# Kernel optimization log

Measured on AMD Instinct MI355X. Metric: run time of the kernel, lower is better.

Reference implementation:

```python
import jax, jax.numpy as jnp
import numpy as np


def _rotary_matrix(m, d):
    """Dense block-diagonal rotary matrix R[m, d, d], faithful to the source
    including the (i-1) exponent quirk."""
    d2 = d // 2
    i = jnp.arange(d2, dtype=jnp.float32)
    theta = 10000.0 ** (-2.0 * (i - 1.0) / d)          # note: (i-1), as in source
    ang = jnp.arange(m, dtype=jnp.float32)[:, None] * theta[None, :]  # [m, d2]
    cos, sin = jnp.cos(ang), jnp.sin(ang)
    ev = 2 * jnp.arange(d2)
    od = ev + 1
    R = jnp.zeros((m, d, d), dtype=jnp.float32)
    R = R.at[:, ev, ev].set(cos)
    R = R.at[:, ev, od].set(-sin)
    R = R.at[:, od, ev].set(sin)
    R = R.at[:, od, od].set(cos)
    return R


def setup_inputs() -> dict:
    key = jax.random.key(0)
    kx, kq, kk, kv = jax.random.split(key, 4)
    B, M, D = 4, 1024, 512
    scale = 1.0 / np.float32(np.sqrt(D))
    x = jax.random.normal(kx, (B, M, D), dtype=jnp.float32)
    w_q = jax.random.normal(kq, (D, D), dtype=jnp.float32) * scale
    w_k = jax.random.normal(kk, (D, D), dtype=jnp.float32) * scale
    w_v = jax.random.normal(kv, (D, D), dtype=jnp.float32) * scale
    R = _rotary_matrix(M, D)  # [M, D, D], ~1 GB, constant (requires_grad=False)
    return {"x": x, "w_q": w_q, "w_k": w_k, "w_v": w_v, "R": R}


def reference(x, w_q, w_k, w_v, R):
    b, m, d = x.shape
    # nn.Linear(d, d, bias=False): y = x @ W.T
    q = jnp.einsum('bmd,ed->bme', x, w_q)
    k = jnp.einsum('bmd,ed->bme', x, w_k)
    v = jnp.einsum('bmd,ed->bme', x, w_v)
    # dense per-position rotary bmm: torch.bmm(q.transpose(0,1), R[:m]).transpose(0,1)
    q_rot = jnp.einsum('bmd,mde->bme', q, R[:m])
    k_rot = jnp.einsum('bmd,mde->bme', k, R[:m])
    # F.scaled_dot_product_attention WITHOUT mask (no is_causal in source);
    # dropout_p=0.1 omitted (deterministic / eval-mode reference)
    scores = jnp.einsum('bqd,bkd->bqk', q_rot, k_rot) / np.float32(np.sqrt(d))
    attn = jax.nn.softmax(scores, axis=-1)
    return jnp.einsum('bqk,bkd->bqd', attn, v)
```

## Files before the change

### kernel.cpp

```cpp
#include <hip/hip_runtime.h>
#include <hip/hip_bf16.h>

#define BB 4
#define MM 1024
#define DD 512
#define MT (BB*MM)

typedef __bf16  bf16x8 __attribute__((ext_vector_type(8)));
typedef float   f32x4  __attribute__((ext_vector_type(4)));

typedef __attribute__((address_space(1))) const unsigned char gas_char;
typedef __attribute__((address_space(3))) unsigned char las_char;

__device__ __forceinline__ void gl_lds16(const void* g, void* l){
    __builtin_amdgcn_global_load_lds((gas_char*)g, (las_char*)l, 16, 0, 0);
}

__device__ __forceinline__ float bf2f(ushort u){
    union{float f; unsigned u;} x; x.u = (unsigned)u << 16; return x.f;
}
__device__ __forceinline__ ushort f2bf(float f){
    union{float f; unsigned u;} x; x.f = f;
    unsigned r = x.u + 0x7FFF + ((x.u >> 16) & 1);
    return (ushort)(r >> 16);
}

__device__ __forceinline__ int detect_bf16(const ushort* __restrict__ x){
    int lane = threadIdx.x & 63;
    ushort u = x[2*lane];
    int e = (u >> 7) & 0xFF;
    bool sane = (e >= 114 && e <= 140);
    unsigned long long b = __ballot(sane);
    return (__popcll(b) >= 48) ? 1 : 0;
}

__device__ __forceinline__ uint4 ld8(const void* __restrict__ base, size_t eidx, int fl){
    if (fl) return ((const uint4*)base)[eidx >> 3];
    const float4* f = (const float4*)base + (eidx >> 2);
    float4 a = f[0], b = f[1];
    uint4 o;
    o.x = (uint)f2bf(a.x) | ((uint)f2bf(a.y) << 16);
    o.y = (uint)f2bf(a.z) | ((uint)f2bf(a.w) << 16);
    o.z = (uint)f2bf(b.x) | ((uint)f2bf(b.y) << 16);
    o.w = (uint)f2bf(b.z) | ((uint)f2bf(b.w) << 16);
    return o;
}

template<int ROWS, int WAVES>
__device__ __forceinline__ void stage_tile(const ushort* __restrict__ g, int ldel,
                                           char* lds, int wid, int lane){
    const int rr = wid*8 + (lane >> 3);
    const int sc = ((lane & 7) ^ (lane >> 3)) * 8;
    #pragma unroll
    for (int r = 0; r < ROWS; r += WAVES*8)
        gl_lds16(g + (size_t)(r + rr)*ldel + sc, lds + (size_t)(r + wid*8)*128);
}

__device__ __forceinline__ bf16x8 frag(const char* lds, int row, int c16){
    return *(const bf16x8*)(lds + row*128 + (((c16) ^ (row & 7)) << 4));
}

__global__ void k_cs(const void* __restrict__ R, const void* __restrict__ x,
                     const void* __restrict__ wq, const void* __restrict__ wk,
                     const void* __restrict__ wv,
                     float2* __restrict__ cs, ushort* __restrict__ xb,
                     ushort* __restrict__ w3b){
    const int fl = detect_bf16((const ushort*)x);
    const int m = blockIdx.x, i = threadIdx.x;
    float c, s;
    if (fl){
        const ushort* Rb = (const ushort*)R;
        size_t base = (size_t)m * DD * DD;
        c = bf2f(Rb[base + (size_t)(2*i)   * DD + 2*i]);
        s = bf2f(Rb[base + (size_t)(2*i+1) * DD + 2*i]);
    } else {
        float ex = -((float)i - 1.0f) * (1.0f/256.0f);
        float th = expf(ex * 9.210340371976184f);
        float ang = (float)m * th;
        c = cosf(ang); s = sinf(ang);
    }
    cs[m*256 + i] = make_float2(c, s);

    size_t chunk = (size_t)m*256 + i;
    ((uint4*)xb)[chunk] = ld8(x, chunk*8, fl);

    if (m < 384){
        const void* W = (m < 128) ? wq : (m < 256) ? wk : wv;
        ushort* dst = w3b + (size_t)(m >> 7) * DD * DD;
        size_t ch = (size_t)(m & 127)*256 + i;
        ((uint4*)dst)[ch] = ld8(W, ch*8, fl);
    }
}

__launch_bounds__(256, 2)
__global__ void k_qkv(const ushort* __restrict__ xb, const ushort* __restrict__ w3b,
                      const float2* __restrict__ cs,
                      ushort* __restrict__ qr, ushort* __restrict__ kr,
                      ushort* __restrict__ vt){
    const int lin = blockIdx.x;
    const int swz = (lin & 7) * 96 + (lin >> 3);
    const int tm  = swz / 24;
    const int rm  = swz % 24;
    const int mat = rm >> 3;
    const int tn  = rm & 7;

    const ushort* A  = xb  + (size_t)(tm*128)*DD;
    const ushort* Bw = w3b + (size_t)mat*DD*DD + (size_t)(tn*64)*DD;

    const int t = threadIdx.x, lane = t & 63, wid = t >> 6;
    const int wr = (wid >> 1)*64, wc = (wid & 1)*32;

    __shared__ char smem[24576];

    f32x4 acc[4][2] = {};

    #pragma unroll 1
    for (int kt = 0; kt < DD/64; ++kt){
        stage_tile<128,4>(A  + kt*64, DD, smem,       wid, lane);
        stage_tile<64,4> (Bw + kt*64, DD, smem+16384, wid, lane);
        __syncthreads();
        #pragma unroll
        for (int kk = 0; kk < 2; ++kk){
            bf16x8 af[4], bv[2];
            #pragma unroll
            for (int i = 0; i < 4; i++)
                af[i] = frag(smem,       wr + i*16 + (lane&15), kk*4 + (lane>>4));
            #pragma unroll
            for (int j = 0; j < 2; j++)
                bv[j] = frag(smem+16384, wc + j*16 + (lane&15), kk*4 + (lane>>4));
            #pragma unroll
            for (int i = 0; i < 4; i++)
                #pragma unroll
                for (int j = 0; j < 2; j++)
                    acc[i][j] = __builtin_amdgcn_mfma_f32_16x16x32_bf16(af[i], bv[j], acc[i][j], 0, 0, 0);
        }
        __syncthreads();
    }

    #pragma unroll
    for (int i = 0; i < 4; i++){
        #pragma unroll
        for (int j = 0; j < 2; j++){
            #pragma unroll
            for (int r = 0; r < 4; r++){
                int row = tm*128 + wr + i*16 + (lane>>4)*4 + r;
                int col = tn*64 + wc + j*16 + (lane&15);
                float v = acc[i][j][r];
                if (mat == 2){
                    vt[((size_t)(row >> 10)*DD + col)*MM + (row & (MM-1))] = f2bf(v);
                } else {
                    float p = __shfl_xor(v, 1);
                    float2 csv = cs[(row & (MM-1))*256 + (col >> 1)];
                    float o = (col & 1) ? (v*csv.x - p*csv.y) : (v*csv.x + p*csv.y);
                    ushort* out = (mat == 0) ? qr : kr;
                    out[(size_t)row*DD + col] = f2bf(o);
                }
            }
        }
    }
}

__launch_bounds__(256, 2)
__global__ void k_sexp(const ushort* __restrict__ qr, const ushort* __restrict__ kr,
                       ushort* __restrict__ Pexp){
    const int lin = blockIdx.x;
    const int swz = (lin & 7) * 64 + (lin >> 3);
    const int b   = swz >> 7;
    const int r7  = swz & 127;
    const int tm  = r7 >> 4;
    const int tn  = r7 & 15;

    const ushort* A  = qr + (size_t)b*MM*DD + (size_t)(tm*128)*DD;
    const ushort* Bm = kr + (size_t)b*MM*DD + (size_t)(tn*64)*DD;
    ushort*      out = Pexp + (size_t)b*MM*MM;
    const float scale = 0.04419417382415922f;

    const int t = threadIdx.x, lane = t & 63, wid = t >> 6;
    const int wr = (wid >> 1)*64, wc = (wid & 1)*32;

    __shared__ char smem[24576];

    f32x4 acc[4][2] = {};

    #pragma unroll 1
    for (int kt = 0; kt < DD/64; ++kt){
        stage_tile<128,4>(A  + kt*64, DD, smem,       wid, lane);
        stage_tile<64,4> (Bm + kt*64, DD, smem+16384, wid, lane);
        __syncthreads();
        #pragma unroll
        for (int kk = 0; kk < 2; ++kk){
            bf16x8 af[4], bv[2];
            #pragma unroll
            for (int i = 0; i < 4; i++)
                af[i] = frag(smem,       wr + i*16 + (lane&15), kk*4 + (lane>>4));
            #pragma unroll
            for (int j = 0; j < 2; j++)
                bv[j] = frag(smem+16384, wc + j*16 + (lane&15), kk*4 + (lane>>4));
            #pragma unroll
            for (int i = 0; i < 4; i++)
                #pragma unroll
                for (int j = 0; j < 2; j++)
                    acc[i][j] = __builtin_amdgcn_mfma_f32_16x16x32_bf16(af[i], bv[j], acc[i][j], 0, 0, 0);
        }
        __syncthreads();
    }

    #pragma unroll
    for (int i = 0; i < 4; i++)
        #pragma unroll
        for (int j = 0; j < 2; j++)
            #pragma unroll
            for (int r = 0; r < 4; r++){
                int row = tm*128 + wr + i*16 + (lane>>4)*4 + r;
                int col = tn*64 + wc + j*16 + (lane&15);
                float e = __expf(acc[i][j][r] * scale - 8.0f);
                out[(size_t)row*MM + col] = f2bf(e);
            }
}

__launch_bounds__(256, 2)
__global__ void k_pv(const ushort* __restrict__ P, const ushort* __restrict__ vt,
                     const ushort* __restrict__ xdet, void* __restrict__ O){
    const int lin = blockIdx.x;
    const int swz = (lin & 7) * 64 + (lin >> 3);
    const int b   = swz >> 7;
    const int r7  = swz & 127;
    const int tm  = r7 >> 3;
    const int tn  = r7 & 7;

    const int fl = detect_bf16(xdet);
    const ushort* A  = P  + ((size_t)b*MM + tm*64) * MM;
    const ushort* Bv = vt + (size_t)b*DD*MM + (size_t)(tn*64)*MM;

    const int t = threadIdx.x, lane = t & 63, wid = t >> 6;
    const int wr = (wid >> 1)*32, wc = (wid & 1)*32;

    __shared__ char smem[16384];

    f32x4 acc[2][2] = {};
    float lsum[2] = {0.0f, 0.0f};

    #pragma unroll 1
    for (int kt = 0; kt < MM/64; ++kt){
        stage_tile<64,4>(A  + kt*64, MM, smem,      wid, lane);
        stage_tile<64,4>(Bv + kt*64, MM, smem+8192, wid, lane);
        __syncthreads();
        #pragma unroll
        for (int kk = 0; kk < 2; ++kk){
            bf16x8 af[2], bv[2];
            #pragma unroll
            for (int i = 0; i < 2; i++){
                af[i] = frag(smem, wr + i*16 + (lane&15), kk*4 + (lane>>4));
                #pragma unroll
                for (int e = 0; e < 8; e++) lsum[i] += (float)af[i][e];
            }
            #pragma unroll
            for (int j = 0; j < 2; j++)
                bv[j] = frag(smem+8192, wc + j*16 + (lane&15), kk*4 + (lane>>4));
            #pragma unroll
            for (int i = 0; i < 2; i++)
                #pragma unroll
                for (int j = 0; j < 2; j++)
                    acc[i][j] = __builtin_amdgcn_mfma_f32_16x16x32_bf16(af[i], bv[j], acc[i][j], 0, 0, 0);
        }
        __syncthreads();
    }

    #pragma unroll
    for (int i = 0; i < 2; i++){
        lsum[i] += __shfl_xor(lsum[i], 16);
        lsum[i] += __shfl_xor(lsum[i], 32);
    }
    float linv[2][4];
    #pragma unroll
    for (int i = 0; i < 2; i++)
        #pragma unroll
        for (int r = 0; r < 4; r++)
            linv[i][r] = 1.0f / __shfl(lsum[i], (lane>>4)*4 + r);

    #pragma unroll
    for (int i = 0; i < 2; i++)
        #pragma unroll
        for (int j = 0; j < 2; j++)
            #pragma unroll
            for (int r = 0; r < 4; r++){
                int row = b*MM + tm*64 + wr + i*16 + (lane>>4)*4 + r;
                int col = tn*64 + wc + j*16 + (lane&15);
                float o = acc[i][j][r] * linv[i][r];
                if (fl) ((ushort*)O)[(size_t)row*DD + col] = f2bf(o);
                else    ((float*) O)[(size_t)row*DD + col] = o;
            }
}

extern "C" void kernel_launch(void* const* d_in, const int* in_sizes, int n_in,
                              void* d_out, int out_size, void* d_ws, size_t ws_size,
                              hipStream_t stream){
    const void* x  = d_in[0];
    const void* wq = d_in[1];
    const void* wk = d_in[2];
    const void* wv = d_in[3];
    const void* R  = d_in[4];

    char* ws = (char*)d_ws;
    float2* cs  = (float2*)ws;
    ushort* xb  = (ushort*)(ws + (2u  << 20));
    ushort* w3b = (ushort*)(ws + (6u  << 20));
    ushort* qr  = (ushort*)(ws + (8u  << 20));
    ushort* kr  = (ushort*)(ws + (12u << 20));
    ushort* vt  = (ushort*)(ws + (16u << 20));
    ushort* Px  = (ushort*)(ws + (20u << 20));

    if (ws_size < (28u << 20)) return;

    k_cs  <<<dim3(MM),  dim3(256), 0, stream>>>(R, x, wq, wk, wv, cs, xb, w3b);
    k_qkv <<<dim3(768), dim3(256), 0, stream>>>(xb, w3b, cs, qr, kr, vt);
    k_sexp<<<dim3(512), dim3(256), 0, stream>>>(qr, kr, Px);
    k_pv  <<<dim3(512), dim3(256), 0, stream>>>(Px, vt, (const ushort*)x, d_out);
}
```

Measured before the change: 57.18 us.

## Widen GEMM K-tile to 128 and flatten conversion kernel grid

The three GEMM kernels now stage 128-wide K slices instead of 64, which halves the number of barrier-separated main-loop iterations and doubles the LDS footprint per block. The staging and fragment-read swizzles are rewritten for a 256-byte row pitch. The prep kernel becomes a flat grid over x conversion, weight conversion and cos/sin generation, so the uneven per-block work goes away. k_qkv launch bounds go from 2 to 3 blocks per SM, which adds register pressure, and the larger LDS use may cap occupancy.

```diff
diff --git a/kernel.cpp b/kernel.cpp
--- a/kernel.cpp
+++ b/kernel.cpp
@@ -46,53 +46,53 @@
     return o;
 }
 
-template<int ROWS, int WAVES>
-__device__ __forceinline__ void stage_tile(const ushort* __restrict__ g, int ldel,
-                                           char* lds, int wid, int lane){
-    const int rr = wid*8 + (lane >> 3);
-    const int sc = ((lane & 7) ^ (lane >> 3)) * 8;
-    #pragma unroll
-    for (int r = 0; r < ROWS; r += WAVES*8)
-        gl_lds16(g + (size_t)(r + rr)*ldel + sc, lds + (size_t)(r + wid*8)*128);
-}
-
-__device__ __forceinline__ bf16x8 frag(const char* lds, int row, int c16){
-    return *(const bf16x8*)(lds + row*128 + (((c16) ^ (row & 7)) << 4));
-}
-
-__global__ void k_cs(const void* __restrict__ R, const void* __restrict__ x,
-                     const void* __restrict__ wq, const void* __restrict__ wk,
-                     const void* __restrict__ wv,
-                     float2* __restrict__ cs, ushort* __restrict__ xb,
-                     ushort* __restrict__ w3b){
+template<int ROWS>
+__device__ __forceinline__ void stage128(const ushort* __restrict__ g, int ldel,
+                                         char* lds, int wid, int lane){
+    const int rr = wid*4 + (lane >> 4);
+    const int sc = (((lane & 15) ^ (rr & 7))) * 8;
+    #pragma unroll
+    for (int r = 0; r < ROWS; r += 16)
+        gl_lds16(g + (size_t)(r + rr)*ldel + sc, lds + (size_t)(r + wid*4)*256);
+}
+
+__device__ __forceinline__ bf16x8 frag128(const char* lds, int row, int c16){
+    return *(const bf16x8*)(lds + row*256 + (((c16) ^ (row & 7)) << 4));
+}
+
+__global__ void k_conv(const void* __restrict__ x,  const void* __restrict__ wq,
+                       const void* __restrict__ wk, const void* __restrict__ wv,
+                       const void* __restrict__ R,
+                       ushort* __restrict__ xb, ushort* __restrict__ w3b,
+                       float2* __restrict__ cs){
     const int fl = detect_bf16((const ushort*)x);
-    const int m = blockIdx.x, i = threadIdx.x;
-    float c, s;
-    if (fl){
-        const ushort* Rb = (const ushort*)R;
-        size_t base = (size_t)m * DD * DD;
-        c = bf2f(Rb[base + (size_t)(2*i)   * DD + 2*i]);
-        s = bf2f(Rb[base + (size_t)(2*i+1) * DD + 2*i]);
+    int idx = blockIdx.x*256 + threadIdx.x;
+    if (idx < 262144){
+        ((uint4*)xb)[idx] = ld8(x, (size_t)idx*8, fl);
+    } else if (idx < 360448){
+        int w = idx - 262144;
+        const void* W = (w < 32768) ? wq : (w < 65536) ? wk : wv;
+        ((uint4*)w3b)[w] = ld8(W, (size_t)(w & 32767)*8, fl);
     } else {
-        float ex = -((float)i - 1.0f) * (1.0f/256.0f);
-        float th = expf(ex * 9.210340371976184f);
-        float ang = (float)m * th;
-        c = cosf(ang); s = sinf(ang);
-    }
-    cs[m*256 + i] = make_float2(c, s);
-
-    size_t chunk = (size_t)m*256 + i;
-    ((uint4*)xb)[chunk] = ld8(x, chunk*8, fl);
-
-    if (m < 384){
-        const void* W = (m < 128) ? wq : (m < 256) ? wk : wv;
-        ushort* dst = w3b + (size_t)(m >> 7) * DD * DD;
-        size_t ch = (size_t)(m & 127)*256 + i;
-        ((uint4*)dst)[ch] = ld8(W, ch*8, fl);
-    }
-}
-
-__launch_bounds__(256, 2)
+        int cidx = idx - 360448;
+        int m = cidx >> 8, i = cidx & 255;
+        float c, s;
+        if (fl){
+            const ushort* Rb = (const ushort*)R;
+            size_t base = (size_t)m * DD * DD;
+            c = bf2f(Rb[base + (size_t)(2*i)   * DD + 2*i]);
+            s = bf2f(Rb[base + (size_t)(2*i+1) * DD + 2*i]);
+        } else {
+            float ex = -((float)i - 1.0f) * (1.0f/256.0f);
+            float th = expf(ex * 9.210340371976184f);
+            float ang = (float)m * th;
+            c = cosf(ang); s = sinf(ang);
+        }
+        cs[cidx] = make_float2(c, s);
+    }
+}
+
+__launch_bounds__(256, 3)
 __global__ void k_qkv(const ushort* __restrict__ xb, const ushort* __restrict__ w3b,
                       const float2* __restrict__ cs,
                       ushort* __restrict__ qr, ushort* __restrict__ kr,
@@ -110,24 +110,24 @@
     const int t = threadIdx.x, lane = t & 63, wid = t >> 6;
     const int wr = (wid >> 1)*64, wc = (wid & 1)*32;
 
-    __shared__ char smem[24576];
+    __shared__ char smem[49152];
 
     f32x4 acc[4][2] = {};
 
     #pragma unroll 1
-    for (int kt = 0; kt < DD/64; ++kt){
-        stage_tile<128,4>(A  + kt*64, DD, smem,       wid, lane);
-        stage_tile<64,4> (Bw + kt*64, DD, smem+16384, wid, lane);
-        __syncthreads();
-        #pragma unroll
-        for (int kk = 0; kk < 2; ++kk){
+    for (int kt = 0; kt < DD/128; ++kt){
+        stage128<128>(A  + kt*128, DD, smem,       wid, lane);
+        stage128<64> (Bw + kt*128, DD, smem+32768, wid, lane);
+        __syncthreads();
+        #pragma unroll
+        for (int kk = 0; kk < 4; ++kk){
             bf16x8 af[4], bv[2];
             #pragma unroll
             for (int i = 0; i < 4; i++)
-                af[i] = frag(smem,       wr + i*16 + (lane&15), kk*4 + (lane>>4));
+                af[i] = frag128(smem,       wr + i*16 + (lane&15), kk*4 + (lane>>4));
             #pragma unroll
             for (int j = 0; j < 2; j++)
-                bv[j] = frag(smem+16384, wc + j*16 + (lane&15), kk*4 + (lane>>4));
+                bv[j] = frag128(smem+32768, wc + j*16 + (lane&15), kk*4 + (lane>>4));
             #pragma unroll
             for (int i = 0; i < 4; i++)
                 #pragma unroll
@@ -178,24 +178,24 @@
     const int t = threadIdx.x, lane = t & 63, wid = t >> 6;
     const int wr = (wid >> 1)*64, wc = (wid & 1)*32;
 
-    __shared__ char smem[24576];
+    __shared__ char smem[49152];
 
     f32x4 acc[4][2] = {};
 
     #pragma unroll 1
-    for (int kt = 0; kt < DD/64; ++kt){
-        stage_tile<128,4>(A  + kt*64, DD, smem,       wid, lane);
-        stage_tile<64,4> (Bm + kt*64, DD, smem+16384, wid, lane);
-        __syncthreads();
-        #pragma unroll
-        for (int kk = 0; kk < 2; ++kk){
+    for (int kt = 0; kt < DD/128; ++kt){
+        stage128<128>(A  + kt*128, DD, smem,       wid, lane);
+        stage128<64> (Bm + kt*128, DD, smem+32768, wid, lane);
+        __syncthreads();
+        #pragma unroll
+        for (int kk = 0; kk < 4; ++kk){
             bf16x8 af[4], bv[2];
             #pragma unroll
             for (int i = 0; i < 4; i++)
-                af[i] = frag(smem,       wr + i*16 + (lane&15), kk*4 + (lane>>4));
+                af[i] = frag128(smem,       wr + i*16 + (lane&15), kk*4 + (lane>>4));
             #pragma unroll
             for (int j = 0; j < 2; j++)
-                bv[j] = frag(smem+16384, wc + j*16 + (lane&15), kk*4 + (lane>>4));
+                bv[j] = frag128(smem+32768, wc + j*16 + (lane&15), kk*4 + (lane>>4));
             #pragma unroll
             for (int i = 0; i < 4; i++)
                 #pragma unroll
@@ -235,28 +235,28 @@
     const int t = threadIdx.x, lane = t & 63, wid = t >> 6;
     const int wr = (wid >> 1)*32, wc = (wid & 1)*32;
 
-    __shared__ char smem[16384];
+    __shared__ char smem[32768];
 
     f32x4 acc[2][2] = {};
     float lsum[2] = {0.0f, 0.0f};
 
     #pragma unroll 1
-    for (int kt = 0; kt < MM/64; ++kt){
-        stage_tile<64,4>(A  + kt*64, MM, smem,      wid, lane);
-        stage_tile<64,4>(Bv + kt*64, MM, smem+8192, wid, lane);
-        __syncthreads();
-        #pragma unroll
-        for (int kk = 0; kk < 2; ++kk){
+    for (int kt = 0; kt < MM/128; ++kt){
+        stage128<64>(A  + kt*128, MM, smem,       wid, lane);
+        stage128<64>(Bv + kt*128, MM, smem+16384, wid, lane);
+        __syncthreads();
+        #pragma unroll
+        for (int kk = 0; kk < 4; ++kk){
             bf16x8 af[2], bv[2];
             #pragma unroll
             for (int i = 0; i < 2; i++){
-                af[i] = frag(smem, wr + i*16 + (lane&15), kk*4 + (lane>>4));
+                af[i] = frag128(smem, wr + i*16 + (lane&15), kk*4 + (lane>>4));
                 #pragma unroll
                 for (int e = 0; e < 8; e++) lsum[i] += (float)af[i][e];
             }
             #pragma unroll
             for (int j = 0; j < 2; j++)
-                bv[j] = frag(smem+8192, wc + j*16 + (lane&15), kk*4 + (lane>>4));
+                bv[j] = frag128(smem+16384, wc + j*16 + (lane&15), kk*4 + (lane>>4));
             #pragma unroll
             for (int i = 0; i < 2; i++)
                 #pragma unroll
@@ -312,8 +312,8 @@
 
     if (ws_size < (28u << 20)) return;
 
-    k_cs  <<<dim3(MM),  dim3(256), 0, stream>>>(R, x, wq, wk, wv, cs, xb, w3b);
-    k_qkv <<<dim3(768), dim3(256), 0, stream>>>(xb, w3b, cs, qr, kr, vt);
-    k_sexp<<<dim3(512), dim3(256), 0, stream>>>(qr, kr, Px);
-    k_pv  <<<dim3(512), dim3(256), 0, stream>>>(Px, vt, (const ushort*)x, d_out);
-}
+    k_conv<<<dim3(2432), dim3(256), 0, stream>>>(x, wq, wk, wv, R, xb, w3b, cs);
+    k_qkv <<<dim3(768),  dim3(256), 0, stream>>>(xb, w3b, cs, qr, kr, vt);
+    k_sexp<<<dim3(512),  dim3(256), 0, stream>>>(qr, kr, Px);
+    k_pv  <<<dim3(512),  dim3(256), 0, stream>>>(Px, vt, (const ushort*)x, d_out);
+}
```

New measurement: 53.86 us. -5.8%, faster.
